# Performance work log

Hardware: AMD Instinct MI355X
Metric: run time of the kernel (lower is better)

The kernel has to match this reference:

```python
import jax, jax.numpy as jnp
import numpy as np

B, L, HSIZE = 16, 512, 1024
H, D = 16, 64  # HHEAD = HSIZE/base, HBASE = 64

def setup_inputs() -> dict:
    key = jax.random.key(0)
    ks = jax.random.split(key, 10)
    inp = {
        'v': jax.random.normal(ks[0], (B, L, HSIZE), jnp.float32),
        'k': jax.random.normal(ks[1], (B, L, HSIZE), jnp.float32),
        'q': jax.random.normal(ks[2], (B, L, HSIZE), jnp.float32),
        'img_abs': jax.random.normal(ks[3], (B, L, HSIZE), jnp.float32),
        'Wv': jax.random.normal(ks[4], (HSIZE, HSIZE), jnp.float32) * 0.02,
        'Wk': jax.random.normal(ks[5], (HSIZE, HSIZE), jnp.float32) * 0.02,
        'Wq': jax.random.normal(ks[6], (HSIZE, HSIZE), jnp.float32) * 0.02,
        'Wm': jax.random.normal(ks[7], (HSIZE, HSIZE), jnp.float32) * 0.02,
        'abs_mask': jax.random.bernoulli(ks[8], 0.1, (B, 1, L, L)),
        'mask': jax.random.bernoulli(ks[9], 0.1, (B, 1, L, L)),
    }
    return inp

def reference(v, k, q, img_abs, Wv, Wk, Wq, Wm, abs_mask, mask):
    nb = q.shape[0]
    # Linear (no bias) then split heads: [B, L, HSIZE] -> [B, H, L, D]
    def heads(x):
        return x.reshape(nb, -1, H, D).transpose(0, 2, 1, 3)
    vh = heads(v @ Wv.T)
    kh = heads(k @ Wk.T)
    qh = heads(q @ Wq.T)
    ph = heads(img_abs)
    scale = 1.0 / jnp.sqrt(jnp.asarray(D, qh.dtype))
    # modulate: attention of q over positional features, residual-added to q
    s1 = jnp.einsum('bhqd,bhpd->bhqp', qh, ph) * scale
    s1 = jnp.where(abs_mask, jnp.asarray(-1e9, s1.dtype), s1)
    qh = qh + jnp.einsum('bhqp,bhpd->bhqd', jax.nn.softmax(s1, axis=-1), ph)
    # main attention (dropout = identity in eval mode)
    s2 = jnp.einsum('bhqd,bhkd->bhqk', qh, kh) * scale
    s2 = jnp.where(mask, jnp.asarray(-1e9, s2.dtype), s2)
    atted = jnp.einsum('bhqk,bhkd->bhqd', jax.nn.softmax(s2, axis=-1), vh)
    atted = atted.transpose(0, 2, 1, 3).reshape(nb, -1, H * D)
    return atted @ Wm.T
```

## Files before the change

kernel.cpp:

```cpp
#include <hip/hip_runtime.h>

typedef unsigned short u16;
typedef unsigned int u32;
typedef unsigned long long u64;
typedef __attribute__((ext_vector_type(8))) short short8;
typedef __attribute__((ext_vector_type(4))) float f32x4;
typedef __attribute__((ext_vector_type(4))) u32 u32x4;

#define NB 16
#define SL 512
#define HS 1024
#define NHEAD 16
#define HD 64
#define NTOKC (16L * 512 * 1024)
#define NWC   (1024L * 1024)
#define NMC   (16L * 512 * 512)

typedef const __attribute__((address_space(1))) u32* gas_t;
typedef __attribute__((address_space(3))) u32* las_t;

__device__ __forceinline__ void gld16(const u16* g, u16* l) {
  __builtin_amdgcn_global_load_lds((gas_t)g, (las_t)l, 16, 0, 0);
}

__device__ __forceinline__ u16 f2bf(float f) {
  union { float f; unsigned u; } c; c.f = f;
  unsigned r = c.u + 0x7FFFu + ((c.u >> 16) & 1u);
  return (u16)(r >> 16);
}
__device__ __forceinline__ float bf2f(u16 u) {
  union { float f; unsigned u; } c; c.u = ((unsigned)u) << 16;
  return c.f;
}
__device__ __forceinline__ u32 cvt_pk_bf16(float a, float b) {
  u32 r;
  asm("v_cvt_pk_bf16_f32 %0, %1, %2" : "=v"(r) : "v"(a), "v"(b));
  return r;
}

__global__ __launch_bounds__(256) void prep(
    const float* __restrict__ v, const float* __restrict__ k,
    const float* __restrict__ q, const float* __restrict__ img,
    const float* __restrict__ Wv, const float* __restrict__ Wk,
    const float* __restrict__ Wq, const float* __restrict__ Wm,
    const int* __restrict__ absm, const int* __restrict__ mask,
    u16* __restrict__ ovk, u16* __restrict__ xq, u16* __restrict__ pb,
    u16* __restrict__ w4, u64* __restrict__ bits) {
  const int y = blockIdx.y;
  const long bx = blockIdx.x;
  if (y < 4) {
    const float* in = y == 0 ? v : y == 1 ? k : y == 2 ? q : img;
    u16* out = y == 0 ? ovk : y == 1 ? ovk + NTOKC : y == 2 ? xq : pb;
    long i = (bx * 256 + threadIdx.x) * 4;
    float4 f = *(const float4*)(in + i);
    uint2 u;
    u.x = (unsigned)f2bf(f.x) | ((unsigned)f2bf(f.y) << 16);
    u.y = (unsigned)f2bf(f.z) | ((unsigned)f2bf(f.w) << 16);
    *(uint2*)(out + i) = u;
  } else if (y == 4) {
    if (bx >= 4096) return;
    long i = bx * 1024 + threadIdx.x * 4;
    int j = (int)(i >> 20);
    const float* in = j == 0 ? Wv : j == 1 ? Wk : j == 2 ? Wq : Wm;
    long off = i & (NWC - 1);
    float4 f = *(const float4*)(in + off);
    uint2 u;
    u.x = (unsigned)f2bf(f.x) | ((unsigned)f2bf(f.y) << 16);
    u.y = (unsigned)f2bf(f.z) | ((unsigned)f2bf(f.w) << 16);
    *(uint2*)(w4 + i) = u;
  } else {
#pragma unroll
    for (int rep = 0; rep < 4; ++rep) {
      long i = (bx * 4 + rep) * 256 + threadIdx.x;
      const int* m = (i >= NMC) ? mask : absm;
      long off = i & (NMC - 1);
      u64 bset = __ballot(m[off] != 0);
      if ((threadIdx.x & 63) == 0) bits[i >> 6] = bset;
    }
  }
}

__global__ __launch_bounds__(256) void gemm_p3(const u16* __restrict__ Avk,
                                               const u16* __restrict__ Aq,
                                               const u16* __restrict__ W4,
                                               u16* __restrict__ Cb) {
  __shared__ u16 As[128 * 64];
  __shared__ u16 Bs[128 * 64];
  const int tid = threadIdx.x;
  const int wave = tid >> 6, lane = tid & 63;
  const int quad = lane >> 4, l16 = lane & 15;
  const int l7 = l16 & 7;
  const int sel = blockIdx.x >> 6;
  const int row0 = (blockIdx.x & 63) * 128, col0 = blockIdx.y * 128;
  const int wm = (wave >> 1) * 64, wn = (wave & 1) * 64;
  const int lrow = lane >> 3;
  const int scb = (lane & 7) ^ lrow;
  const int K = HS, N = HS;

  const u16* A = (sel == 2) ? Aq : Avk + (long)sel * NTOKC;
  const u16* W = W4 + (long)sel * NWC;
  u16* C = Cb + (long)sel * NTOKC;

  f32x4 acc[4][4];
#pragma unroll
  for (int mt = 0; mt < 4; ++mt)
#pragma unroll
    for (int nt = 0; nt < 4; ++nt) acc[mt][nt] = (f32x4){0.f, 0.f, 0.f, 0.f};

  const u16* Ab = A + (long)row0 * K;
  const u16* Wb = W + (long)col0 * K;

  for (int k0 = 0; k0 < K; k0 += 64) {
    __syncthreads();
#pragma unroll
    for (int it = 0; it < 4; ++it) {
      int seg = wave * 4 + it;
      int r = seg * 8 + lrow;
      gld16(Ab + (long)r * K + k0 + scb * 8, As + seg * 512);
      gld16(Wb + (long)r * K + k0 + scb * 8, Bs + seg * 512);
    }
    __syncthreads();
#pragma unroll
    for (int kt = 0; kt < 2; ++kt) {
      short8 af[4], bw[4];
#pragma unroll
      for (int mt = 0; mt < 4; ++mt)
        af[mt] = *(const short8*)(As + (wm + mt * 16 + l16) * 64 +
                                  (((kt * 4 + quad) ^ l7) * 8));
#pragma unroll
      for (int nt = 0; nt < 4; ++nt)
        bw[nt] = *(const short8*)(Bs + (wn + nt * 16 + l16) * 64 +
                                  (((kt * 4 + quad) ^ l7) * 8));
#pragma unroll
      for (int mt = 0; mt < 4; ++mt)
#pragma unroll
        for (int nt = 0; nt < 4; ++nt)
          acc[mt][nt] = __builtin_amdgcn_mfma_f32_16x16x32_bf16(
              af[mt], bw[nt], acc[mt][nt], 0, 0, 0);
    }
  }
#pragma unroll
  for (int mt = 0; mt < 4; ++mt)
#pragma unroll
    for (int nt = 0; nt < 4; ++nt)
#pragma unroll
      for (int i = 0; i < 4; ++i) {
        long r = row0 + wm + mt * 16 + quad * 4 + i;
        long c = col0 + wn + nt * 16 + l16;
        C[r * N + c] = f2bf(acc[mt][nt][i]);
      }
}

__global__ __launch_bounds__(256) void gemm_f(const u16* __restrict__ A,
                                              const u16* __restrict__ W,
                                              float* __restrict__ C) {
  __shared__ u16 As[128 * 64];
  __shared__ u16 Bs[128 * 64];
  const int tid = threadIdx.x;
  const int wave = tid >> 6, lane = tid & 63;
  const int quad = lane >> 4, l16 = lane & 15;
  const int l7 = l16 & 7;
  const int row0 = blockIdx.x * 128, col0 = blockIdx.y * 128;
  const int wm = (wave >> 1) * 64, wn = (wave & 1) * 64;
  const int lrow = lane >> 3;
  const int scb = (lane & 7) ^ lrow;
  const int K = HS, N = HS;

  f32x4 acc[4][4];
#pragma unroll
  for (int mt = 0; mt < 4; ++mt)
#pragma unroll
    for (int nt = 0; nt < 4; ++nt) acc[mt][nt] = (f32x4){0.f, 0.f, 0.f, 0.f};

  const u16* Ab = A + (long)row0 * K;
  const u16* Wb = W + (long)col0 * K;

  for (int k0 = 0; k0 < K; k0 += 64) {
    __syncthreads();
#pragma unroll
    for (int it = 0; it < 4; ++it) {
      int seg = wave * 4 + it;
      int r = seg * 8 + lrow;
      gld16(Ab + (long)r * K + k0 + scb * 8, As + seg * 512);
      gld16(Wb + (long)r * K + k0 + scb * 8, Bs + seg * 512);
    }
    __syncthreads();
#pragma unroll
    for (int kt = 0; kt < 2; ++kt) {
      short8 af[4], bw[4];
#pragma unroll
      for (int mt = 0; mt < 4; ++mt)
        af[mt] = *(const short8*)(As + (wm + mt * 16 + l16) * 64 +
                                  (((kt * 4 + quad) ^ l7) * 8));
#pragma unroll
      for (int nt = 0; nt < 4; ++nt)
        bw[nt] = *(const short8*)(Bs + (wn + nt * 16 + l16) * 64 +
                                  (((kt * 4 + quad) ^ l7) * 8));
#pragma unroll
      for (int mt = 0; mt < 4; ++mt)
#pragma unroll
        for (int nt = 0; nt < 4; ++nt)
          acc[mt][nt] = __builtin_amdgcn_mfma_f32_16x16x32_bf16(
              af[mt], bw[nt], acc[mt][nt], 0, 0, 0);
    }
  }
#pragma unroll
  for (int mt = 0; mt < 4; ++mt)
#pragma unroll
    for (int nt = 0; nt < 4; ++nt)
#pragma unroll
      for (int i = 0; i < 4; ++i) {
        long r = row0 + wm + mt * 16 + quad * 4 + i;
        long c = col0 + wn + nt * 16 + l16;
        C[r * N + c] = acc[mt][nt][i];
      }
}

template <bool SAME>
__device__ __forceinline__ void attn_stage(
    const u16* __restrict__ Kb, const u16* __restrict__ Vb,
    const u64* __restrict__ Mb, int qrow, short8 qf[2], float& l_p,
    f32x4 o[4], u16 (*Ks)[72], u16 (*Vs)[72],
    int quad, int l16, int sr, int sds, int vcol) {
  u64 mall[8];
#pragma unroll
  for (int t = 0; t < 8; ++t) mall[t] = Mb[(long)qrow * 8 + t];
  uint4 kp = *(const uint4*)(Kb + (long)sr * HS + sds);
  uint4 vp;
  if (!SAME) vp = *(const uint4*)(Vb + (long)sr * HS + sds);
  {
    *(uint4*)&Ks[sr][sds] = kp;
    union { uint4 q; u16 e[8]; } tv;
    tv.q = SAME ? kp : vp;
#pragma unroll
    for (int j = 0; j < 8; ++j) Vs[sds + j][vcol] = tv.e[j];
  }
  __syncthreads();
  for (int t = 0; t < 8; ++t) {
    const int cur = t & 1;
    if (t < 7) {
      kp = *(const uint4*)(Kb + (long)((t + 1) * 64 + sr) * HS + sds);
      if (!SAME)
        vp = *(const uint4*)(Vb + (long)((t + 1) * 64 + sr) * HS + sds);
    }
    u16(*Kc)[72] = Ks + cur * 64;
    u16(*Vc)[72] = Vs + cur * 64;
    f32x4 s[4];
#pragma unroll
    for (int nt = 0; nt < 4; ++nt) s[nt] = (f32x4){0.f, 0.f, 0.f, 0.f};
#pragma unroll
    for (int kt = 0; kt < 2; ++kt)
#pragma unroll
      for (int nt = 0; nt < 4; ++nt) {
        short8 ak = *(const short8*)&Kc[nt * 16 + l16][kt * 32 + quad * 8];
        s[nt] = __builtin_amdgcn_mfma_f32_16x16x32_bf16(ak, qf[kt], s[nt],
                                                        0, 0, 0);
      }
    const u64 mw = mall[t];
    u32 pk[8];
    float lp = 0.f;
#pragma unroll
    for (int nt = 0; nt < 4; ++nt) {
      const u32 mb = (u32)(mw >> (nt * 16 + quad * 4));
#pragma unroll
      for (int ih = 0; ih < 2; ++ih) {
        float p0 = (mb & (1u << (2 * ih))) ? 0.f
                                           : __expf(s[nt][2 * ih] * 0.125f);
        float p1 = (mb & (1u << (2 * ih + 1)))
                       ? 0.f
                       : __expf(s[nt][2 * ih + 1] * 0.125f);
        lp += p0 + p1;
        pk[nt * 2 + ih] = cvt_pk_bf16(p0, p1);
      }
    }
    l_p += lp;
#pragma unroll
    for (int kt = 0; kt < 2; ++kt) {
      u32x4 av;
#pragma unroll
      for (int j2 = 0; j2 < 4; ++j2) {
        int src = ((quad & 1) * 2 + (j2 >> 1)) * 16 + l16;
        u32 vlo = (u32)__shfl((int)pk[(2 * kt) * 2 + (j2 & 1)], src, 64);
        u32 vhi = (u32)__shfl((int)pk[(2 * kt + 1) * 2 + (j2 & 1)], src, 64);
        av[j2] = (quad & 2) ? vhi : vlo;
      }
      union { u32x4 u; short8 s8; } cv;
      cv.u = av;
#pragma unroll
      for (int nt = 0; nt < 4; ++nt) {
        short8 bv = *(const short8*)&Vc[nt * 16 + l16]
                                      [(kt * 32 + quad * 8) ^ ((nt & 3) << 4)];
        o[nt] = __builtin_amdgcn_mfma_f32_16x16x32_bf16(cv.s8, bv, o[nt],
                                                        0, 0, 0);
      }
    }
    if (t < 7) {
      u16(*Kn)[72] = Ks + (cur ^ 1) * 64;
      u16(*Vn)[72] = Vs + (cur ^ 1) * 64;
      *(uint4*)&Kn[sr][sds] = kp;
      union { uint4 q; u16 e[8]; } tv;
      tv.q = SAME ? kp : vp;
#pragma unroll
      for (int j = 0; j < 8; ++j) Vn[sds + j][vcol] = tv.e[j];
      __syncthreads();
    }
  }
}

__global__ __launch_bounds__(512, 4) void attn_fused(
    const u16* __restrict__ Qp, const u16* __restrict__ Pbp,
    const u16* __restrict__ Kp, const u16* __restrict__ Vp,
    const u64* __restrict__ B0, const u64* __restrict__ B1,
    u16* __restrict__ Op) {
  __shared__ u16 Ks[128][72];
  __shared__ u16 Vs[128][72];
  const int tid = threadIdx.x;
  const int wave = tid >> 6, lane = tid & 63;
  const int quad = lane >> 4, l16 = lane & 15;
  const int qt = blockIdx.x, h = blockIdx.y, b = blockIdx.z;
  const int q0 = qt * 128;
  const long bs = (long)SL * HS;
  const u16* Qb = Qp + (long)b * bs + h * HD;
  const u16* Pb = Pbp + (long)b * bs + h * HD;
  const u16* Kb = Kp + (long)b * bs + h * HD;
  const u16* Vb = Vp + (long)b * bs + h * HD;
  const u64* M0 = B0 + (long)b * SL * 8;
  const u64* M1 = B1 + (long)b * SL * 8;
  const int sr = tid >> 3, sds = (tid & 7) * 8;
  const int vcol = sr ^ (((sds >> 4) & 3) << 4);
  const int qrow = q0 + wave * 16 + l16;

  short8 qf[2];
#pragma unroll
  for (int kt = 0; kt < 2; ++kt)
    qf[kt] = *(const short8*)(Qb + (long)qrow * HS + kt * 32 + quad * 8);

  float l_p = 0.f;
  f32x4 o[4];
#pragma unroll
  for (int nt = 0; nt < 4; ++nt) o[nt] = (f32x4){0.f, 0.f, 0.f, 0.f};

  attn_stage<true>(Pb, Pb, M0, qrow, qf, l_p, o, Ks, Vs, quad, l16, sr, sds,
                   vcol);

  {
    float rs = l_p;
    rs += __shfl_xor(rs, 16, 64);
    rs += __shfl_xor(rs, 32, 64);
    float inv = 1.f / rs;
    float invq[4];
#pragma unroll
    for (int i = 0; i < 4; ++i) invq[i] = __shfl(inv, quad * 4 + i, 64);
    __syncthreads();
#pragma unroll
    for (int i = 0; i < 4; ++i)
#pragma unroll
      for (int nt = 0; nt < 4; ++nt)
        Ks[wave * 16 + quad * 4 + i][nt * 16 + l16] =
            f2bf(o[nt][i] * invq[i]);
#pragma unroll
    for (int kt = 0; kt < 2; ++kt) {
      short8 t8 = *(const short8*)&Ks[wave * 16 + l16][kt * 32 + quad * 8];
#pragma unroll
      for (int j = 0; j < 8; ++j)
        qf[kt][j] = (short)f2bf(bf2f((u16)t8[j]) + bf2f((u16)qf[kt][j]));
    }
#pragma unroll
    for (int nt = 0; nt < 4; ++nt) o[nt] = (f32x4){0.f, 0.f, 0.f, 0.f};
    l_p = 0.f;
    __syncthreads();
  }

  attn_stage<false>(Kb, Vb, M1, qrow, qf, l_p, o, Ks, Vs, quad, l16, sr, sds,
                    vcol);

  {
    float rs = l_p;
    rs += __shfl_xor(rs, 16, 64);
    rs += __shfl_xor(rs, 32, 64);
    float inv = 1.f / rs;
    float invq[4];
#pragma unroll
    for (int i = 0; i < 4; ++i) invq[i] = __shfl(inv, quad * 4 + i, 64);
    u16* Ob = Op + (long)b * bs + h * HD;
#pragma unroll
    for (int i = 0; i < 4; ++i) {
      int r = q0 + wave * 16 + quad * 4 + i;
#pragma unroll
      for (int nt = 0; nt < 4; ++nt)
        Ob[(long)r * HS + nt * 16 + l16] = f2bf(o[nt][i] * invq[i]);
    }
  }
}

extern "C" void kernel_launch(void* const* d_in, const int* in_sizes, int n_in,
                              void* d_out, int out_size, void* d_ws,
                              size_t ws_size, hipStream_t stream) {
  const float* v   = (const float*)d_in[0];
  const float* k   = (const float*)d_in[1];
  const float* q   = (const float*)d_in[2];
  const float* img = (const float*)d_in[3];
  const float* Wv  = (const float*)d_in[4];
  const float* Wk  = (const float*)d_in[5];
  const float* Wq  = (const float*)d_in[6];
  const float* Wm  = (const float*)d_in[7];
  const int* absm  = (const int*)d_in[8];
  const int* mask  = (const int*)d_in[9];
  float* out = (float*)d_out;

  const long NTOK = NTOKC;
  const long NW   = NWC;
  const long NM   = NMC;
  u16* ovk = (u16*)d_out;
  u16* ws  = (u16*)d_ws;
  u16* xq  = ws;
  u16* pb  = ws + 1 * NTOK;
  u16* vh  = ws + 2 * NTOK;
  u16* kh  = ws + 3 * NTOK;
  u16* qh  = ws + 4 * NTOK;
  u16* w4  = ws + 5 * NTOK;
  u64* bt0 = (u64*)(w4 + 4 * NW);
  u64* bt1 = bt0 + NM / 64;
  u16* att = xq;

  prep<<<dim3(8192, 6), 256, 0, stream>>>(v, k, q, img, Wv, Wk, Wq, Wm,
                                          absm, mask, ovk, xq, pb, w4, bt0);
  gemm_p3<<<dim3(192, 8), 256, 0, stream>>>(ovk, xq, w4, vh);
  attn_fused<<<dim3(SL / 128, NHEAD, NB), 512, 0, stream>>>(
      qh, pb, kh, vh, bt0, bt1, att);
  gemm_f<<<dim3(NB * SL / 128, HS / 128), 256, 0, stream>>>(att, w4 + 3 * NW,
                                                            out);
}
```

Before: 381.7 us.

## Process all 512 query rows per block to reuse staged K/V tiles

Each attention block now handles a whole (head, batch) pair, 4 query tiles of 128 rows, instead of one 128-row tile. K/V (and positional) tiles staged into shared memory are then reused across four query groups, cutting global K/V traffic by four. Mask words are now prefetched one tile ahead rather than loaded all at once. In exchange the grid shrinks to 256 blocks, and register pressure rises from the 4x larger accumulator and Q fragment arrays, so launch bounds drop to 2 blocks per CU. That risks occupancy and leaves fewer blocks to spread across the CUs.

After: 371.6 us. -2.6%, faster.

```diff
diff --git a/kernel.cpp b/kernel.cpp
--- a/kernel.cpp
+++ b/kernel.cpp
@@ -219,15 +219,15 @@
 template <bool SAME>
 __device__ __forceinline__ void attn_stage(
     const u16* __restrict__ Kb, const u16* __restrict__ Vb,
-    const u64* __restrict__ Mb, int qrow, short8 qf[2], float& l_p,
-    f32x4 o[4], u16 (*Ks)[72], u16 (*Vs)[72],
+    const u64* __restrict__ Mb, int qbase, short8 qf[4][2], float l_p[4],
+    f32x4 o[4][4], u16 (*Ks)[72], u16 (*Vs)[72],
     int quad, int l16, int sr, int sds, int vcol) {
-  u64 mall[8];
-#pragma unroll
-  for (int t = 0; t < 8; ++t) mall[t] = Mb[(long)qrow * 8 + t];
   uint4 kp = *(const uint4*)(Kb + (long)sr * HS + sds);
   uint4 vp;
   if (!SAME) vp = *(const uint4*)(Vb + (long)sr * HS + sds);
+  u64 mcur[4], mnxt[4];
+#pragma unroll
+  for (int p = 0; p < 4; ++p) mcur[p] = Mb[(long)(qbase + p * 128) * 8];
   {
     *(uint4*)&Ks[sr][sds] = kp;
     union { uint4 q; u16 e[8]; } tv;
@@ -242,56 +242,68 @@
       kp = *(const uint4*)(Kb + (long)((t + 1) * 64 + sr) * HS + sds);
       if (!SAME)
         vp = *(const uint4*)(Vb + (long)((t + 1) * 64 + sr) * HS + sds);
+#pragma unroll
+      for (int p = 0; p < 4; ++p)
+        mnxt[p] = Mb[(long)(qbase + p * 128) * 8 + t + 1];
     }
     u16(*Kc)[72] = Ks + cur * 64;
     u16(*Vc)[72] = Vs + cur * 64;
-    f32x4 s[4];
-#pragma unroll
-    for (int nt = 0; nt < 4; ++nt) s[nt] = (f32x4){0.f, 0.f, 0.f, 0.f};
+    short8 ak[2][4], bv[2][4];
 #pragma unroll
     for (int kt = 0; kt < 2; ++kt)
 #pragma unroll
       for (int nt = 0; nt < 4; ++nt) {
-        short8 ak = *(const short8*)&Kc[nt * 16 + l16][kt * 32 + quad * 8];
-        s[nt] = __builtin_amdgcn_mfma_f32_16x16x32_bf16(ak, qf[kt], s[nt],
-                                                        0, 0, 0);
+        ak[kt][nt] = *(const short8*)&Kc[nt * 16 + l16][kt * 32 + quad * 8];
+        bv[kt][nt] = *(const short8*)&Vc[nt * 16 + l16]
+                                       [(kt * 32 + quad * 8) ^ ((nt & 3) << 4)];
       }
-    const u64 mw = mall[t];
-    u32 pk[8];
-    float lp = 0.f;
-#pragma unroll
-    for (int nt = 0; nt < 4; ++nt) {
-      const u32 mb = (u32)(mw >> (nt * 16 + quad * 4));
-#pragma unroll
-      for (int ih = 0; ih < 2; ++ih) {
-        float p0 = (mb & (1u << (2 * ih))) ? 0.f
-                                           : __expf(s[nt][2 * ih] * 0.125f);
-        float p1 = (mb & (1u << (2 * ih + 1)))
-                       ? 0.f
-                       : __expf(s[nt][2 * ih + 1] * 0.125f);
-        lp += p0 + p1;
-        pk[nt * 2 + ih] = cvt_pk_bf16(p0, p1);
+#pragma unroll
+    for (int p = 0; p < 4; ++p) {
+      f32x4 s[4];
+#pragma unroll
+      for (int nt = 0; nt < 4; ++nt) s[nt] = (f32x4){0.f, 0.f, 0.f, 0.f};
+#pragma unroll
+      for (int kt = 0; kt < 2; ++kt)
+#pragma unroll
+        for (int nt = 0; nt < 4; ++nt)
+          s[nt] = __builtin_amdgcn_mfma_f32_16x16x32_bf16(ak[kt][nt],
+                                                          qf[p][kt], s[nt],
+                                                          0, 0, 0);
+      const u64 mw = mcur[p];
+      u32 pk[8];
+      float lp = 0.f;
+#pragma unroll
+      for (int nt = 0; nt < 4; ++nt) {
+        const u32 mb = (u32)(mw >> (nt * 16 + quad * 4));
+#pragma unroll
+        for (int ih = 0; ih < 2; ++ih) {
+          float p0 = (mb & (1u << (2 * ih)))
+                         ? 0.f
+                         : __expf(s[nt][2 * ih] * 0.125f);
+          float p1 = (mb & (1u << (2 * ih + 1)))
+                         ? 0.f
+                         : __expf(s[nt][2 * ih + 1] * 0.125f);
+          lp += p0 + p1;
+          pk[nt * 2 + ih] = cvt_pk_bf16(p0, p1);
+        }
       }
-    }
-    l_p += lp;
-#pragma unroll
-    for (int kt = 0; kt < 2; ++kt) {
-      u32x4 av;
-#pragma unroll
-      for (int j2 = 0; j2 < 4; ++j2) {
-        int src = ((quad & 1) * 2 + (j2 >> 1)) * 16 + l16;
-        u32 vlo = (u32)__shfl((int)pk[(2 * kt) * 2 + (j2 & 1)], src, 64);
-        u32 vhi = (u32)__shfl((int)pk[(2 * kt + 1) * 2 + (j2 & 1)], src, 64);
-        av[j2] = (quad & 2) ? vhi : vlo;
-      }
-      union { u32x4 u; short8 s8; } cv;
-      cv.u = av;
-#pragma unroll
-      for (int nt = 0; nt < 4; ++nt) {
-        short8 bv = *(const short8*)&Vc[nt * 16 + l16]
-                                      [(kt * 32 + quad * 8) ^ ((nt & 3) << 4)];
-        o[nt] = __builtin_amdgcn_mfma_f32_16x16x32_bf16(cv.s8, bv, o[nt],
-                                                        0, 0, 0);
+      l_p[p] += lp;
+#pragma unroll
+      for (int kt = 0; kt < 2; ++kt) {
+        u32x4 av;
+#pragma unroll
+        for (int j2 = 0; j2 < 4; ++j2) {
+          int src = ((quad & 1) * 2 + (j2 >> 1)) * 16 + l16;
+          u32 vlo = (u32)__shfl((int)pk[(2 * kt) * 2 + (j2 & 1)], src, 64);
+          u32 vhi = (u32)__shfl((int)pk[(2 * kt + 1) * 2 + (j2 & 1)], src, 64);
+          av[j2] = (quad & 2) ? vhi : vlo;
+        }
+        union { u32x4 u; short8 s8; } cv;
+        cv.u = av;
+#pragma unroll
+        for (int nt = 0; nt < 4; ++nt)
+          o[p][nt] = __builtin_amdgcn_mfma_f32_16x16x32_bf16(
+              cv.s8, bv[kt][nt], o[p][nt], 0, 0, 0);
       }
     }
     if (t < 7) {
@@ -302,12 +314,14 @@
       tv.q = SAME ? kp : vp;
 #pragma unroll
       for (int j = 0; j < 8; ++j) Vn[sds + j][vcol] = tv.e[j];
+#pragma unroll
+      for (int p = 0; p < 4; ++p) mcur[p] = mnxt[p];
       __syncthreads();
     }
   }
 }
 
-__global__ __launch_bounds__(512, 4) void attn_fused(
+__global__ __launch_bounds__(512, 2) void attn_fused(
     const u16* __restrict__ Qp, const u16* __restrict__ Pbp,
     const u16* __restrict__ Kp, const u16* __restrict__ Vp,
     const u64* __restrict__ B0, const u64* __restrict__ B1,
@@ -317,8 +331,7 @@
   const int tid = threadIdx.x;
   const int wave = tid >> 6, lane = tid & 63;
   const int quad = lane >> 4, l16 = lane & 15;
-  const int qt = blockIdx.x, h = blockIdx.y, b = blockIdx.z;
-  const int q0 = qt * 128;
+  const int h = blockIdx.x, b = blockIdx.y;
   const long bs = (long)SL * HS;
   const u16* Qb = Qp + (long)b * bs + h * HD;
   const u16* Pb = Pbp + (long)b * bs + h * HD;
@@ -328,67 +341,74 @@
   const u64* M1 = B1 + (long)b * SL * 8;
   const int sr = tid >> 3, sds = (tid & 7) * 8;
   const int vcol = sr ^ (((sds >> 4) & 3) << 4);
-  const int qrow = q0 + wave * 16 + l16;
-
-  short8 qf[2];
-#pragma unroll
-  for (int kt = 0; kt < 2; ++kt)
-    qf[kt] = *(const short8*)(Qb + (long)qrow * HS + kt * 32 + quad * 8);
-
-  float l_p = 0.f;
-  f32x4 o[4];
-#pragma unroll
-  for (int nt = 0; nt < 4; ++nt) o[nt] = (f32x4){0.f, 0.f, 0.f, 0.f};
-
-  attn_stage<true>(Pb, Pb, M0, qrow, qf, l_p, o, Ks, Vs, quad, l16, sr, sds,
+  const int qbase = wave * 16 + l16;
+
+  short8 qf[4][2];
+#pragma unroll
+  for (int p = 0; p < 4; ++p)
+#pragma unroll
+    for (int kt = 0; kt < 2; ++kt)
+      qf[p][kt] = *(const short8*)(Qb + (long)(p * 128 + qbase) * HS +
+                                   kt * 32 + quad * 8);
+
+  float l_p[4] = {0.f, 0.f, 0.f, 0.f};
+  f32x4 o[4][4];
+#pragma unroll
+  for (int p = 0; p < 4; ++p)
+#pragma unroll
+    for (int nt = 0; nt < 4; ++nt) o[p][nt] = (f32x4){0.f, 0.f, 0.f, 0.f};
+
+  attn_stage<true>(Pb, Pb, M0, qbase, qf, l_p, o, Ks, Vs, quad, l16, sr, sds,
                    vcol);
 
-  {
-    float rs = l_p;
+  __syncthreads();
+#pragma unroll
+  for (int p = 0; p < 4; ++p) {
+    float rs = l_p[p];
     rs += __shfl_xor(rs, 16, 64);
     rs += __shfl_xor(rs, 32, 64);
     float inv = 1.f / rs;
     float invq[4];
 #pragma unroll
     for (int i = 0; i < 4; ++i) invq[i] = __shfl(inv, quad * 4 + i, 64);
-    __syncthreads();
 #pragma unroll
     for (int i = 0; i < 4; ++i)
 #pragma unroll
       for (int nt = 0; nt < 4; ++nt)
         Ks[wave * 16 + quad * 4 + i][nt * 16 + l16] =
-            f2bf(o[nt][i] * invq[i]);
+            f2bf(o[p][nt][i] * invq[i]);
 #pragma unroll
     for (int kt = 0; kt < 2; ++kt) {
       short8 t8 = *(const short8*)&Ks[wave * 16 + l16][kt * 32 + quad * 8];
 #pragma unroll
       for (int j = 0; j < 8; ++j)
-        qf[kt][j] = (short)f2bf(bf2f((u16)t8[j]) + bf2f((u16)qf[kt][j]));
-    }
-#pragma unroll
-    for (int nt = 0; nt < 4; ++nt) o[nt] = (f32x4){0.f, 0.f, 0.f, 0.f};
-    l_p = 0.f;
-    __syncthreads();
-  }
-
-  attn_stage<false>(Kb, Vb, M1, qrow, qf, l_p, o, Ks, Vs, quad, l16, sr, sds,
+        qf[p][kt][j] = (short)f2bf(bf2f((u16)t8[j]) + bf2f((u16)qf[p][kt][j]));
+    }
+#pragma unroll
+    for (int nt = 0; nt < 4; ++nt) o[p][nt] = (f32x4){0.f, 0.f, 0.f, 0.f};
+    l_p[p] = 0.f;
+  }
+  __syncthreads();
+
+  attn_stage<false>(Kb, Vb, M1, qbase, qf, l_p, o, Ks, Vs, quad, l16, sr, sds,
                     vcol);
 
-  {
-    float rs = l_p;
+  u16* Ob = Op + (long)b * bs + h * HD;
+#pragma unroll
+  for (int p = 0; p < 4; ++p) {
+    float rs = l_p[p];
     rs += __shfl_xor(rs, 16, 64);
     rs += __shfl_xor(rs, 32, 64);
     float inv = 1.f / rs;
     float invq[4];
 #pragma unroll
     for (int i = 0; i < 4; ++i) invq[i] = __shfl(inv, quad * 4 + i, 64);
-    u16* Ob = Op + (long)b * bs + h * HD;
 #pragma unroll
     for (int i = 0; i < 4; ++i) {
-      int r = q0 + wave * 16 + quad * 4 + i;
+      int r = p * 128 + wave * 16 + quad * 4 + i;
 #pragma unroll
       for (int nt = 0; nt < 4; ++nt)
-        Ob[(long)r * HS + nt * 16 + l16] = f2bf(o[nt][i] * invq[i]);
+        Ob[(long)r * HS + nt * 16 + l16] = f2bf(o[p][nt][i] * invq[i]);
     }
   }
 }
@@ -426,7 +446,7 @@
   prep<<<dim3(8192, 6), 256, 0, stream>>>(v, k, q, img, Wv, Wk, Wq, Wm,
                                           absm, mask, ovk, xq, pb, w4, bt0);
   gemm_p3<<<dim3(192, 8), 256, 0, stream>>>(ovk, xq, w4, vh);
-  attn_fused<<<dim3(SL / 128, NHEAD, NB), 512, 0, stream>>>(
+  attn_fused<<<dim3(NHEAD, NB), 512, 0, stream>>>(
       qh, pb, kh, vh, bt0, bt1, att);
   gemm_f<<<dim3(NB * SL / 128, HS / 128), 256, 0, stream>>>(att, w4 + 3 * NW,
                                                             out);
```
